# Kernel tuning notes

Hardware: AMD Instinct MI355X
Metric: run time of the kernel (lower is better)

Reference implementation:

```python
import jax, jax.numpy as jnp
import numpy as np

# config (from LLObjectCondensation defaults)
Q_MIN = 0.5
S_B = 1.0
POT_SCALE = 1.0
REP_SCALE = 1.0
BETA_SCALE = 1.0
K_MAX = 128  # max objects per event; truth id 0 == noise


def setup_inputs() -> dict:
    key = jax.random.key(0)
    k1, k2, k3 = jax.random.split(key, 3)
    B, N, C = 8, 40000, 2
    ccoords = jax.random.normal(k1, (B, N, C), dtype=jnp.float32)
    beta = jax.random.uniform(k2, (B, N), dtype=jnp.float32, minval=1e-3, maxval=1.0 - 1e-3)
    t_idx = jax.random.randint(k3, (B, N), 0, K_MAX, dtype=jnp.int32)
    return {"ccoords": ccoords, "beta": beta, "t_idx": t_idx}


def reference(ccoords, beta, t_idx):
    B, N, C = ccoords.shape
    K = K_MAX
    beta_c = jnp.clip(beta, 1e-6, 1.0 - 1e-5)
    # charge q = arctanh^2(beta) + q_min
    q = jnp.arctanh(beta_c / 1.002) ** 2 + Q_MIN  # [B,N]

    obj_ids = jnp.arange(K, dtype=t_idx.dtype)
    M = t_idx[:, :, None] == obj_ids  # [B,N,K] hit-belongs-to-object mask
    is_noise = t_idx == 0  # [B,N]
    obj_present = jnp.any(M, axis=1) & (obj_ids > 0)  # [B,K]

    # condensation point alpha_k = argmax beta among hits of object k
    beta_m = jnp.where(M, beta_c[:, :, None], -1.0)  # [B,N,K]
    alpha = jnp.argmax(beta_m, axis=1)  # [B,K]
    x_alpha = jnp.take_along_axis(
        ccoords, jnp.broadcast_to(alpha[:, :, None], (B, K, C)), axis=1
    )  # [B,K,C]
    q_alpha = jnp.take_along_axis(q, alpha, axis=1)  # [B,K]
    beta_alpha = jnp.take_along_axis(beta_c, alpha, axis=1)  # [B,K]

    # pairwise squared distances hit <-> condensation point, via GEMM form
    xn2 = jnp.sum(ccoords * ccoords, axis=-1)  # [B,N]
    xa2 = jnp.sum(x_alpha * x_alpha, axis=-1)  # [B,K]
    d2 = xn2[:, :, None] + xa2[:, None, :] - 2.0 * jnp.einsum(
        "bnc,bkc->bnk", ccoords, x_alpha
    )
    d2 = jnp.maximum(d2, 0.0)
    d = jnp.sqrt(d2 + 1e-6)

    qq = q[:, :, None] * q_alpha[:, None, :]  # [B,N,K]
    pm = obj_present[:, None, :]
    # attractive: same-object hits pulled to condensation point
    V_attr = jnp.sum(jnp.where(M & pm, d2 * qq, 0.0), axis=(1, 2)) / N  # [B]
    # repulsive: other hits pushed away inside unit radius (hinge)
    V_rep = jnp.sum(
        jnp.where((~M) & pm, jnp.maximum(0.0, 1.0 - d) * qq, 0.0), axis=(1, 2)
    ) / N  # [B]

    n_obj = jnp.maximum(jnp.sum(obj_present, axis=-1), 1)
    L_beta = jnp.sum(jnp.where(obj_present, 1.0 - beta_alpha, 0.0), axis=-1) / n_obj
    n_noise = jnp.maximum(jnp.sum(is_noise, axis=-1), 1)
    L_noise = S_B * jnp.sum(jnp.where(is_noise, beta_c, 0.0), axis=-1) / n_noise

    loss = jnp.mean(
        POT_SCALE * V_attr + REP_SCALE * V_rep + BETA_SCALE * (L_beta + L_noise)
    )
    return loss
```

## Files before the change

kernel.cpp:

```cpp
#include <hip/hip_runtime.h>

#define KOBJ  128
#define QMIN  0.5f
#define SB    1.0f
#define BDIM  256
#define NSCB  128
#define BATCH 8
#define PPB   256

typedef unsigned long long u64;
typedef unsigned int u32;


__device__ __forceinline__ float waveRedF(float v) {
    #pragma unroll
    for (int o = 32; o; o >>= 1) v += __shfl_down(v, o, 64);
    return v;
}
__device__ __forceinline__ u32 waveRedU(u32 v) {
    #pragma unroll
    for (int o = 32; o; o >>= 1) v += __shfl_down(v, o, 64);
    return v;
}

__global__ void __launch_bounds__(BDIM)
oc_scan(const float* __restrict__ beta, const int* __restrict__ t_idx,
        u64* __restrict__ pkey, float* __restrict__ nsp, u32* __restrict__ ncp,
        float* __restrict__ out, int N) {
    const int tid = threadIdx.x;
    const int b   = blockIdx.y;
    const int sub = blockIdx.x;
    const int bid = b * NSCB + sub;
    const int chunk = (N + NSCB - 1) / NSCB;
    const int n0 = sub * chunk;
    const int n1 = min(n0 + chunk, N);

    if (bid == 0 && tid == 0) out[0] = 0.f;

    __shared__ u64 skey[KOBJ];
    if (tid < KOBJ) skey[tid] = 0ull;
    __syncthreads();

    float ns = 0.f;
    u32 nc = 0u;
    for (int n = n0 + tid; n < n1; n += BDIM) {
        const float bc = fminf(fmaxf(beta[(size_t)b * N + n], 1e-6f), 1.0f - 1e-5f);
        const int t = t_idx[(size_t)b * N + n];
        const u64 kk = ((u64)__float_as_uint(bc) << 32) | (u64)(~(u32)n);
        atomicMax(&skey[t], kk);
        if (t == 0) { ns += bc; nc++; }
    }
    __syncthreads();
    if (tid < KOBJ) pkey[(size_t)bid * KOBJ + tid] = skey[tid];

    ns = waveRedF(ns);
    nc = waveRedU(nc);
    __shared__ float s_ns[BDIM / 64];
    __shared__ u32   s_nc[BDIM / 64];
    if ((tid & 63) == 0) { s_ns[tid >> 6] = ns; s_nc[tid >> 6] = nc; }
    __syncthreads();
    if (tid == 0) {
        float a = 0.f; u32 c = 0u;
        #pragma unroll
        for (int w = 0; w < BDIM / 64; ++w) { a += s_ns[w]; c += s_nc[w]; }
        nsp[bid] = a; ncp[bid] = c;
    }
}

__global__ void __launch_bounds__(KOBJ)
oc_reduce(const float* __restrict__ cc, const u64* __restrict__ pkey,
          const float* __restrict__ nsp, const u32* __restrict__ ncp,
          float4* __restrict__ xaq, float* __restrict__ qsum,
          float* __restrict__ out, int N) {
    const int b = blockIdx.x;
    const int k = threadIdx.x;

    u64 kv = 0ull;
    #pragma unroll 8
    for (int s = 0; s < NSCB; ++s) {
        const u64 v = pkey[(size_t)(b * NSCB + s) * KOBJ + k];
        kv = v > kv ? v : kv;
    }
    const bool present = (kv != 0ull) && (k > 0);
    float x = 0.f, y = 0.f, qv = 0.f, lb = 0.f;
    u32 pc = 0u;
    if (kv != 0ull) {
        const u32 na = ~(u32)(kv & 0xFFFFFFFFull);
        const float ba = __uint_as_float((u32)(kv >> 32));
        const float2 xy = *(const float2*)&cc[((size_t)b * N + na) * 2];
        x = xy.x; y = xy.y;
        const float a = atanhf(ba / 1.002f);
        qv = a * a + QMIN;
        if (present) { lb = 1.f - ba; pc = 1u; }
    }
    const float qe = present ? qv : 0.f;
    xaq[(size_t)b * KOBJ + k] = make_float4(x, y, qe, 0.f);

    float ns = nsp[b * NSCB + k];
    u32   nc = ncp[b * NSCB + k];

    lb = waveRedF(lb);  pc = waveRedU(pc);
    ns = waveRedF(ns);  nc = waveRedU(nc);
    float qs = waveRedF(qe);
    __shared__ float s_lb[2], s_ns[2], s_qs[2];
    __shared__ u32   s_pc[2], s_nc[2];
    const int wv = k >> 6;
    if ((k & 63) == 0) { s_lb[wv] = lb; s_pc[wv] = pc; s_ns[wv] = ns; s_nc[wv] = nc; s_qs[wv] = qs; }
    __syncthreads();
    if (k == 0) {
        const float L = s_lb[0] + s_lb[1];
        const u32   P = s_pc[0] + s_pc[1];
        const float A = s_ns[0] + s_ns[1];
        const u32   C = s_nc[0] + s_nc[1];
        qsum[b] = s_qs[0] + s_qs[1];
        const float terms = L / (float)max(P, 1u) + SB * A / (float)max(C, 1u);
        atomicAdd(out, terms * (1.f / (float)BATCH));
    }
}

__global__ void __launch_bounds__(PPB)
oc_pairs(const float* __restrict__ cc, const float* __restrict__ beta,
         const int* __restrict__ t_idx,
         const float4* __restrict__ xaq, const float* __restrict__ qsum,
         float* __restrict__ out, int N, float invNB) {
    const int tid = threadIdx.x;
    const int b   = blockIdx.y;
    const int sub = blockIdx.x;
    const int n   = sub * PPB + tid;

    const float4* __restrict__ tab = xaq + (size_t)b * KOBJ;

    float acc_tot = 0.f;
    if (n < N) {
        const float2 xy = *(const float2*)&cc[((size_t)b * N + n) * 2];
        const float bc = fminf(fmaxf(beta[(size_t)b * N + n], 1e-6f), 1.0f - 1e-5f);
        const int t = t_idx[(size_t)b * N + n];
        const float a = atanhf(bc / 1.002f);
        const float qn = a * a + QMIN;
        float acc = 0.f;
        #pragma unroll 8
        for (int k = 0; k < KOBJ; ++k) {
            const float4 T = tab[k];
            const float dx = xy.x - T.x;
            const float dy = xy.y - T.y;
            const float d2e = fmaf(dy, dy, fmaf(dx, dx, 1e-6f));
            const float d = sqrtf(d2e);
            acc = fmaf(T.z, fminf(d, 1.f), acc);
        }
        const float4 Tt = tab[t];
        const float dxt = xy.x - Tt.x;
        const float dyt = xy.y - Tt.y;
        const float d2et = fmaf(dyt, dyt, fmaf(dxt, dxt, 1e-6f));
        const float dt = sqrtf(d2et);
        const float point = qsum[b] - acc + Tt.z * ((d2et - 1e-6f) - 1.f + fminf(dt, 1.f));
        acc_tot = point * qn;
    }

    acc_tot = waveRedF(acc_tot);
    __shared__ float s_a[PPB / 64];
    if ((tid & 63) == 0) s_a[tid >> 6] = acc_tot;
    __syncthreads();
    if (tid == 0) {
        float s = 0.f;
        #pragma unroll
        for (int w = 0; w < PPB / 64; ++w) s += s_a[w];
        atomicAdd(out, s * invNB);
    }
}

extern "C" void kernel_launch(void* const* d_in, const int* in_sizes, int n_in,
                              void* d_out, int out_size, void* d_ws, size_t ws_size,
                              hipStream_t stream) {
    const float* cc   = (const float*)d_in[0];
    const float* beta = (const float*)d_in[1];
    const int*   tix  = (const int*)d_in[2];
    float* out = (float*)d_out;
    const int N = in_sizes[1] / BATCH;

    char* ws = (char*)d_ws;
    u64*    pkey = (u64*)(ws + 0);
    float*  nsp  = (float*)(ws + 1048576);
    u32*    ncp  = (u32*)(ws + 1052672);
    float4* xaq  = (float4*)(ws + 1056768);
    float*  qsum = (float*)(ws + 1073152);

    const int nppb = (N + PPB - 1) / PPB;
    const float invNB = 1.f / ((float)N * (float)BATCH);

    oc_scan  <<<dim3(NSCB, BATCH), BDIM, 0, stream>>>(beta, tix, pkey, nsp, ncp, out, N);
    oc_reduce<<<dim3(BATCH), KOBJ, 0, stream>>>(cc, pkey, nsp, ncp, xaq, qsum, out, N);
    oc_pairs <<<dim3(nppb, BATCH), PPB, 0, stream>>>(cc, beta, tix, xaq, qsum, out, N, invNB);
}
```

Measured before the change: 42.73 us.

## Process two hits per thread with packed float2 math over SoA object table

```diff
diff --git a/kernel.cpp b/kernel.cpp
--- a/kernel.cpp
+++ b/kernel.cpp
@@ -6,10 +6,10 @@
 #define BDIM  256
 #define NSCB  128
 #define BATCH 8
-#define PPB   256
 
 typedef unsigned long long u64;
 typedef unsigned int u32;
+typedef float v2f __attribute__((ext_vector_type(2)));
 
 
 __device__ __forceinline__ float waveRedF(float v) {
@@ -71,6 +71,7 @@
 oc_reduce(const float* __restrict__ cc, const u64* __restrict__ pkey,
           const float* __restrict__ nsp, const u32* __restrict__ ncp,
           float4* __restrict__ xaq, float* __restrict__ qsum,
+          float4* __restrict__ txy2, float2* __restrict__ tq2,
           float* __restrict__ out, int N) {
     const int b = blockIdx.x;
     const int k = threadIdx.x;
@@ -96,6 +97,15 @@
     const float qe = present ? qv : 0.f;
     xaq[(size_t)b * KOBJ + k] = make_float4(x, y, qe, 0.f);
 
+    __shared__ float sx[KOBJ], sy[KOBJ], sq[KOBJ];
+    sx[k] = x; sy[k] = y; sq[k] = qe;
+    __syncthreads();
+    if (k < KOBJ / 2) {
+        txy2[(size_t)b * (KOBJ / 2) + k] =
+            make_float4(sx[2 * k], sx[2 * k + 1], sy[2 * k], sy[2 * k + 1]);
+        tq2[(size_t)b * (KOBJ / 2) + k] = make_float2(sq[2 * k], sq[2 * k + 1]);
+    }
+
     float ns = nsp[b * NSCB + k];
     u32   nc = ncp[b * NSCB + k];
 
@@ -118,52 +128,85 @@
     }
 }
 
-__global__ void __launch_bounds__(PPB)
+__global__ void __launch_bounds__(BDIM)
 oc_pairs(const float* __restrict__ cc, const float* __restrict__ beta,
          const int* __restrict__ t_idx,
-         const float4* __restrict__ xaq, const float* __restrict__ qsum,
+         const float4* __restrict__ xaq,
+         const float4* __restrict__ txy2, const float2* __restrict__ tq2,
+         const float* __restrict__ qsum,
          float* __restrict__ out, int N, float invNB) {
     const int tid = threadIdx.x;
     const int b   = blockIdx.y;
     const int sub = blockIdx.x;
-    const int n   = sub * PPB + tid;
-
-    const float4* __restrict__ tab = xaq + (size_t)b * KOBJ;
-
-    float acc_tot = 0.f;
-    if (n < N) {
-        const float2 xy = *(const float2*)&cc[((size_t)b * N + n) * 2];
-        const float bc = fminf(fmaxf(beta[(size_t)b * N + n], 1e-6f), 1.0f - 1e-5f);
-        const int t = t_idx[(size_t)b * N + n];
-        const float a = atanhf(bc / 1.002f);
-        const float qn = a * a + QMIN;
-        float acc = 0.f;
-        #pragma unroll 8
-        for (int k = 0; k < KOBJ; ++k) {
-            const float4 T = tab[k];
-            const float dx = xy.x - T.x;
-            const float dy = xy.y - T.y;
-            const float d2e = fmaf(dy, dy, fmaf(dx, dx, 1e-6f));
-            const float d = sqrtf(d2e);
-            acc = fmaf(T.z, fminf(d, 1.f), acc);
-        }
-        const float4 Tt = tab[t];
-        const float dxt = xy.x - Tt.x;
-        const float dyt = xy.y - Tt.y;
-        const float d2et = fmaf(dyt, dyt, fmaf(dxt, dxt, 1e-6f));
-        const float dt = sqrtf(d2et);
-        const float point = qsum[b] - acc + Tt.z * ((d2et - 1e-6f) - 1.f + fminf(dt, 1.f));
-        acc_tot = point * qn;
-    }
-
-    acc_tot = waveRedF(acc_tot);
-    __shared__ float s_a[PPB / 64];
-    if ((tid & 63) == 0) s_a[tid >> 6] = acc_tot;
+    const int na  = sub * (BDIM * 2) + tid;
+    const int nb  = na + BDIM;
+
+    const float4* __restrict__ Txy = txy2 + (size_t)b * (KOBJ / 2);
+    const float2* __restrict__ Tq  = tq2  + (size_t)b * (KOBJ / 2);
+    const float qs = qsum[b];
+
+    const bool va = (na < N), vb = (nb < N);
+    const float2 xya = va ? *(const float2*)&cc[((size_t)b * N + na) * 2] : make_float2(0.f, 0.f);
+    const float2 xyb = vb ? *(const float2*)&cc[((size_t)b * N + nb) * 2] : make_float2(0.f, 0.f);
+
+    const v2f pax = {xya.x, xya.x}, pay = {xya.y, xya.y};
+    const v2f pbx = {xyb.x, xyb.x}, pby = {xyb.y, xyb.y};
+    const v2f one2 = {1.f, 1.f}, eps2 = {1e-6f, 1e-6f};
+    v2f acca = {0.f, 0.f}, accb = {0.f, 0.f};
+
+    #pragma unroll 8
+    for (int j = 0; j < KOBJ / 2; ++j) {
+        const float4 T = Txy[j];
+        const float2 Q = Tq[j];
+        const v2f tx = {T.x, T.y};
+        const v2f ty = {T.z, T.w};
+        const v2f qq = {Q.x, Q.y};
+        const v2f dxa = pax - tx, dya = pay - ty;
+        const v2f d2a = dya * dya + (dxa * dxa + eps2);
+        const v2f da  = __builtin_elementwise_sqrt(d2a);
+        acca = acca + qq * __builtin_elementwise_min(da, one2);
+        const v2f dxb = pbx - tx, dyb = pby - ty;
+        const v2f d2b = dyb * dyb + (dxb * dxb + eps2);
+        const v2f db  = __builtin_elementwise_sqrt(d2b);
+        accb = accb + qq * __builtin_elementwise_min(db, one2);
+    }
+
+    float tot = 0.f;
+    if (va) {
+        const float bc = fminf(fmaxf(beta[(size_t)b * N + na], 1e-6f), 1.0f - 1e-5f);
+        const float aa = atanhf(bc / 1.002f);
+        const float qn = aa * aa + QMIN;
+        const int   t  = t_idx[(size_t)b * N + na];
+        const float4 Tt = xaq[(size_t)b * KOBJ + t];
+        const float dxt = xya.x - Tt.x, dyt = xya.y - Tt.y;
+        const float d2e = fmaf(dyt, dyt, fmaf(dxt, dxt, 1e-6f));
+        const float dt  = sqrtf(d2e);
+        const float point = qs - (acca.x + acca.y)
+                          + Tt.z * ((d2e - 1e-6f) - 1.f + fminf(dt, 1.f));
+        tot += point * qn;
+    }
+    if (vb) {
+        const float bc = fminf(fmaxf(beta[(size_t)b * N + nb], 1e-6f), 1.0f - 1e-5f);
+        const float aa = atanhf(bc / 1.002f);
+        const float qn = aa * aa + QMIN;
+        const int   t  = t_idx[(size_t)b * N + nb];
+        const float4 Tt = xaq[(size_t)b * KOBJ + t];
+        const float dxt = xyb.x - Tt.x, dyt = xyb.y - Tt.y;
+        const float d2e = fmaf(dyt, dyt, fmaf(dxt, dxt, 1e-6f));
+        const float dt  = sqrtf(d2e);
+        const float point = qs - (accb.x + accb.y)
+                          + Tt.z * ((d2e - 1e-6f) - 1.f + fminf(dt, 1.f));
+        tot += point * qn;
+    }
+
+    tot = waveRedF(tot);
+    __shared__ float s_a[BDIM / 64];
+    if ((tid & 63) == 0) s_a[tid >> 6] = tot;
     __syncthreads();
     if (tid == 0) {
         float s = 0.f;
         #pragma unroll
-        for (int w = 0; w < PPB / 64; ++w) s += s_a[w];
+        for (int w = 0; w < BDIM / 64; ++w) s += s_a[w];
         atomicAdd(out, s * invNB);
     }
 }
@@ -183,11 +226,14 @@
     u32*    ncp  = (u32*)(ws + 1052672);
     float4* xaq  = (float4*)(ws + 1056768);
     float*  qsum = (float*)(ws + 1073152);
-
-    const int nppb = (N + PPB - 1) / PPB;
+    float4* txy2 = (float4*)(ws + 1073184);
+    float2* tq2  = (float2*)(ws + 1081376);
+
+    const int nppb = (N + BDIM * 2 - 1) / (BDIM * 2);
     const float invNB = 1.f / ((float)N * (float)BATCH);
 
     oc_scan  <<<dim3(NSCB, BATCH), BDIM, 0, stream>>>(beta, tix, pkey, nsp, ncp, out, N);
-    oc_reduce<<<dim3(BATCH), KOBJ, 0, stream>>>(cc, pkey, nsp, ncp, xaq, qsum, out, N);
-    oc_pairs <<<dim3(nppb, BATCH), PPB, 0, stream>>>(cc, beta, tix, xaq, qsum, out, N, invNB);
-}
+    oc_reduce<<<dim3(BATCH), KOBJ, 0, stream>>>(cc, pkey, nsp, ncp, xaq, qsum, txy2, tq2, out, N);
+    oc_pairs <<<dim3(nppb, BATCH), BDIM, 0, stream>>>(cc, beta, tix, xaq, txy2, tq2, qsum,
+                                                      out, N, invNB);
+}
```

Measured after the change: 49.52 us. 15.9% more time.
